# Kernel tuning notes

Hardware: AMD Instinct MI355X
Metric: run time of the kernel (lower is better)

The kernel has to match this reference:

```python
import jax, jax.numpy as jnp
from jax import lax
import numpy as np

TAU_R = 1.0
TAU_W = 5.0
W_MIN, W_MAX = 0.0, 0.05
N_MBON, N_FBN, N_DAN, N_KC = 20, 60, 20, 200
N_RECUR = N_MBON + N_FBN + N_DAN
B, T = 256, 61


def setup_inputs() -> dict:
    key = jax.random.key(0)
    ks = jax.random.split(key, 8)
    r_kc = jax.random.uniform(ks[0], (B, N_KC, T), dtype=jnp.float32)
    r_ext = jax.random.uniform(ks[1], (B, 2, T), dtype=jnp.float32)
    time = jnp.arange(T, dtype=jnp.float32) * 0.5  # dt = 0.5
    # KC->MBON plastic weights start at the max value (0.05), as in init
    W0_W = jax.random.uniform(ks[2], (B, N_MBON, N_KC), dtype=jnp.float32) * W_MAX
    W0_w = jax.random.uniform(ks[3], (B, N_MBON, N_KC), dtype=jnp.float32) * W_MAX
    sqrt2 = np.sqrt(2.0)
    W_mbon = jax.random.normal(ks[4], (N_RECUR, N_MBON)) * np.sqrt(1.0 / (sqrt2 * N_MBON))
    W_fbn = jax.random.normal(ks[5], (N_RECUR, N_FBN)) * np.sqrt(1.0 / (sqrt2 * N_FBN))
    W_dan = jax.random.normal(ks[6], (N_RECUR, N_DAN)) * np.sqrt(1.0 / (sqrt2 * N_DAN))
    W_recur = jnp.concatenate([W_mbon, W_fbn, W_dan], axis=1).astype(jnp.float32)
    W_ext = jax.random.normal(ks[7], (N_FBN, 2), dtype=jnp.float32)
    bias = jnp.full((N_RECUR,), 0.1, dtype=jnp.float32)
    W_readout = jax.random.normal(jax.random.fold_in(key, 99), (1, N_MBON), dtype=jnp.float32) / np.sqrt(N_MBON)
    return {"r_kc": r_kc, "r_ext": r_ext, "time": time, "n_batch": B,
            "W0_W": W0_W, "W0_w": W0_w, "W_recur": W_recur, "W_ext": W_ext,
            "bias": bias, "W_readout": W_readout}


def reference(r_kc, r_ext, time, n_batch, W0_W, W0_w, W_recur, W_ext, bias, W_readout):
    n_mbon, n_kc = W0_W.shape[1], W0_W.shape[2]
    n_fbn = W_ext.shape[0]
    n_recur = W_recur.shape[0]
    n_dan = n_recur - n_mbon - n_fbn
    nb = r_kc.shape[0]
    dt = time[1] - time[0]

    # initial state: FBN/DAN at 0.1, MBON at 0
    r_init = jnp.full((nb, n_recur), 0.1, dtype=r_kc.dtype).at[:, :n_mbon].set(0.0)
    # DAN->MBON weights are zeroed
    Wr = W_recur.at[:n_mbon, -n_dan:].set(0.0)
    rbk0 = r_kc[:, :, 0]            # KC eligibility trace
    rbd0 = r_init[:, -n_dan:]       # DAN eligibility trace
    readout0 = jnp.einsum('om,bm->bo', W_readout, r_init[:, :n_mbon]).squeeze(-1)
    zeros_dan = jnp.zeros((nb, n_dan), dtype=r_kc.dtype)

    def step(carry, xs):
        r, W, wt, rbk, rbd = carry
        rk_t, re_t = xs                                   # [B,n_kc], [B,n_ext]
        I_kc = jnp.einsum('bmk,bk->bm', W, rk_t)          # KC -> MBON via plastic W
        I_fbn = jnp.einsum('fe,be->bf', W_ext, re_t)      # context -> FBN
        I_tot = jnp.concatenate([I_kc, I_fbn, zeros_dan], axis=1)
        Wr_prod = jnp.einsum('sr,br->bs', Wr, r)
        dr = (-r + jax.nn.relu(Wr_prod + bias + I_tot)) / TAU_R
        r_new = r + dr * dt
        # plasticity update (uses the *new* DAN activity)
        rbk_new = rbk + (rk_t - rbk) * dt / TAU_W
        r_dan = r_new[:, -n_dan:]
        rbd_new = rbd + (r_dan - rbd) * dt / TAU_W
        dw = (jnp.einsum('bd,bk->bdk', rbd_new, rk_t)
              - jnp.einsum('bd,bk->bdk', r_dan, rbk_new))
        wt_new = wt + dw * dt
        W_new = jnp.clip(W + (-W + wt_new) / TAU_W * dt, W_MIN, W_MAX)
        ro = jnp.einsum('om,bm->bo', W_readout, r_new[:, :n_mbon]).squeeze(-1)
        return (r_new, W_new, wt_new, rbk_new, rbd_new), (r_new, W_new, wt_new, ro)

    xs = (jnp.moveaxis(r_kc, 2, 0)[:-1], jnp.moveaxis(r_ext, 2, 0)[:-1])
    carry0 = (r_init, W0_W, W0_w, rbk0, rbd0)
    _, (r_s, W_s, wt_s, ro_s) = lax.scan(step, carry0, xs)
    r_series = jnp.concatenate([r_init[None], r_s], axis=0)    # [T,B,n_recur]
    W_series = jnp.concatenate([W0_W[None], W_s], axis=0)      # [T,B,n_mbon,n_kc]
    wt_series = jnp.concatenate([W0_w[None], wt_s], axis=0)    # [T,B,n_mbon,n_kc]
    readout = jnp.concatenate([readout0[None], ro_s], axis=0)  # [T,B]
    return r_series, W_series, wt_series, readout
```

## Files before the change

kernel.cpp:

```cpp
#include <hip/hip_runtime.h>


#define NKC   200
#define NREC  100
#define TSTEP 61
#define NSTEP 60
#define WRSTR 108
#define PSTR  52
#define NTHR  512

typedef float vfloat4 __attribute__((ext_vector_type(4)));

__device__ __forceinline__ void bar_lds() {
    __builtin_amdgcn_sched_barrier(0);
    asm volatile("s_waitcnt lgkmcnt(0)");
    __builtin_amdgcn_s_barrier();
    __builtin_amdgcn_sched_barrier(0);
}

__device__ __forceinline__ void nt_store4(float* p, float4 v) {
    vfloat4 t;
    t.x = v.x; t.y = v.y; t.z = v.z; t.w = v.w;
    __builtin_nontemporal_store(t, (vfloat4*)p);
}
__device__ __forceinline__ void nt_store1(float* p, float v) {
    __builtin_nontemporal_store(v, p);
}

__global__ __launch_bounds__(NTHR, 1) void cond_rnn_kernel(
    const float* __restrict__ r_kc, const float* __restrict__ r_ext,
    const float* __restrict__ timev, const float* __restrict__ W0_W,
    const float* __restrict__ W0_w, const float* __restrict__ W_recur,
    const float* __restrict__ W_ext, const float* __restrict__ bias,
    const float* __restrict__ W_readout, float* __restrict__ out, int B)
{
    int b = blockIdx.x;
    if ((B & 7) == 0) {
        const int cpx = B >> 3;
        b = (blockIdx.x & 7) * cpx + (blockIdx.x >> 3);
    }
    const int tid = threadIdx.x;
    const float dt  = timev[1] - timev[0];
    const float dtw = dt / 5.0f;

    __shared__ __align__(16) float s_rk[TSTEP * NKC];
    __shared__ __align__(16) float s_re[128];
    __shared__ __align__(16) float s_Wr[NREC * WRSTR];
    __shared__ __align__(16) float s_Wro[32];
    __shared__ __align__(16) float s_r[2][112];
    __shared__ __align__(16) float s_rbd[32];
    __shared__ __align__(16) float s_part[20 * PSTR];

    const float* rk_b = r_kc + (size_t)b * (NKC * TSTEP);
    for (int f = tid; f < NKC * TSTEP; f += NTHR) {
        int k = f / TSTEP, t = f - k * TSTEP;
        s_rk[t * NKC + k] = rk_b[f];
    }
    const float* re_b = r_ext + (size_t)b * (2 * TSTEP);
    if (tid < 2 * TSTEP) s_re[tid] = re_b[tid];
    for (int f = tid; f < NREC * NREC; f += NTHR) {
        int s = f / NREC, j = f - s * NREC;
        float v = W_recur[f];
        if (s < 20 && j >= 80) v = 0.f;
        s_Wr[s * WRSTR + j] = v;
    }
    if (tid < 20)  s_Wro[tid] = W_readout[tid];
    if (tid < 100) s_r[0][tid] = (tid < 20) ? 0.f : 0.1f;
    if (tid < 20)  s_rbd[tid] = 0.1f;

    float my_bias = 0.f, we0 = 0.f, we1 = 0.f;
    if (tid < 100) my_bias = bias[tid];
    if (tid >= 20 && tid < 80) { we0 = W_ext[(tid - 20) * 2]; we1 = W_ext[(tid - 20) * 2 + 1]; }
    float rbd_mine = 0.1f;
    float r_mine   = (tid < 20) ? 0.f : 0.1f;

    float* out_r  = out;
    float* out_W  = out + (size_t)TSTEP * B * 100;
    float* out_wt = out_W + (size_t)TSTEP * B * 4000;
    float* out_ro = out_wt + (size_t)TSTEP * B * 4000;

    float4 Wreg[2], wtreg[2], rbkreg[2], rkc[2];
    const float* W0Wb = W0_W + (size_t)b * 4000;
    const float* W0wb = W0_w + (size_t)b * 4000;
    #pragma unroll
    for (int i = 0; i < 2; ++i) {
        int c = tid + NTHR * i;
        if (c < 1000) {
            Wreg[i]  = *(const float4*)(W0Wb + 4 * c);
            wtreg[i] = *(const float4*)(W0wb + 4 * c);
            nt_store4(out_W  + (size_t)b * 4000 + 4 * c, Wreg[i]);
            nt_store4(out_wt + (size_t)b * 4000 + 4 * c, wtreg[i]);
        }
    }
    if (tid < 100) nt_store1(out_r + (size_t)b * 100 + tid, r_mine);

    __syncthreads();

    #pragma unroll
    for (int i = 0; i < 2; ++i) {
        int c = tid + NTHR * i;
        if (c < 1000) {
            int k0 = (4 * c) % NKC;
            int m  = c / 50;
            float4 rk0 = *(const float4*)(s_rk + k0);
            rbkreg[i] = rk0;
            rkc[i]    = rk0;
            float4 w = Wreg[i];
            s_part[m * PSTR + (c % 50)] =
                w.x * rk0.x + w.y * rk0.y + w.z * rk0.z + w.w * rk0.w;
        }
    }
    if (tid == 255) {
        float ro = 0.f;
        #pragma unroll
        for (int mm = 0; mm < 20; ++mm) ro += s_Wro[mm] * s_r[0][mm];
        nt_store1(out_ro + b, ro);
    }
    __syncthreads();

    for (int it = 0; it < NSTEP; ++it) {
        const int cur = it & 1, nxt = cur ^ 1;

        if (tid < 100) {
            float acc = my_bias;
            if (tid < 20) {
                const float* pp = s_part + tid * PSTR;
                #pragma unroll
                for (int q4 = 0; q4 < 12; ++q4) {
                    float4 p4 = *(const float4*)(pp + 4 * q4);
                    acc += p4.x + p4.y + p4.z + p4.w;
                }
                acc += pp[48] + pp[49];
            } else if (tid < 80) {
                acc = fmaf(we0, s_re[it], acc);
                acc = fmaf(we1, s_re[TSTEP + it], acc);
            }
            const float* wr = s_Wr + tid * WRSTR;
            #pragma unroll
            for (int j4 = 0; j4 < 25; ++j4) {
                float4 w4 = *(const float4*)(wr + 4 * j4);
                float4 r4 = *(const float4*)(&s_r[cur][4 * j4]);
                acc = fmaf(w4.x, r4.x, acc); acc = fmaf(w4.y, r4.y, acc);
                acc = fmaf(w4.z, r4.z, acc); acc = fmaf(w4.w, r4.w, acc);
            }
            float drive = acc > 0.f ? acc : 0.f;
            float rn = r_mine + dt * (drive - r_mine);
            r_mine = rn;
            s_r[nxt][tid] = rn;
            nt_store1(out_r + (size_t)(it + 1) * B * 100 + (size_t)b * 100 + tid, rn);
            if (tid >= 80) {
                rbd_mine += (rn - rbd_mine) * dtw;
                s_rbd[tid - 80] = rbd_mine;
            }
        }
        bar_lds();

        float* oW  = out_W  + (size_t)(it + 1) * B * 4000 + (size_t)b * 4000;
        float* owt = out_wt + (size_t)(it + 1) * B * 4000 + (size_t)b * 4000;
        const float* rk_nx  = s_rk + (it + 1) * NKC;
        #pragma unroll
        for (int i = 0; i < 2; ++i) {
            int c = tid + NTHR * i;
            if (c < 1000) {
                int k0 = (4 * c) % NKC;
                int m  = c / 50;
                float4 rk4 = rkc[i];
                float4 rkn = *(const float4*)(rk_nx + k0);
                rkc[i] = rkn;
                float rbdn = s_rbd[m];
                float rdan = s_r[nxt][80 + m];
                float4 rb = rbkreg[i];
                rb.x += (rk4.x - rb.x) * dtw;  rb.y += (rk4.y - rb.y) * dtw;
                rb.z += (rk4.z - rb.z) * dtw;  rb.w += (rk4.w - rb.w) * dtw;
                rbkreg[i] = rb;
                float4 wt = wtreg[i];
                wt.x = fmaf(rbdn * rk4.x - rdan * rb.x, dt, wt.x);
                wt.y = fmaf(rbdn * rk4.y - rdan * rb.y, dt, wt.y);
                wt.z = fmaf(rbdn * rk4.z - rdan * rb.z, dt, wt.z);
                wt.w = fmaf(rbdn * rk4.w - rdan * rb.w, dt, wt.w);
                wtreg[i] = wt;
                float4 w = Wreg[i];
                w.x += (wt.x - w.x) * dtw;  w.y += (wt.y - w.y) * dtw;
                w.z += (wt.z - w.z) * dtw;  w.w += (wt.w - w.w) * dtw;
                w.x = fminf(fmaxf(w.x, 0.f), 0.05f);
                w.y = fminf(fmaxf(w.y, 0.f), 0.05f);
                w.z = fminf(fmaxf(w.z, 0.f), 0.05f);
                w.w = fminf(fmaxf(w.w, 0.f), 0.05f);
                Wreg[i] = w;
                s_part[m * PSTR + (c % 50)] =
                    w.x * rkn.x + w.y * rkn.y + w.z * rkn.z + w.w * rkn.w;
                nt_store4(owt + 4 * c, wt);
                nt_store4(oW  + 4 * c, w);
            }
        }
        if (tid == 255) {
            float ro = 0.f;
            #pragma unroll
            for (int mm = 0; mm < 20; ++mm) ro += s_Wro[mm] * s_r[nxt][mm];
            nt_store1(out_ro + (size_t)(it + 1) * B + b, ro);
        }
        bar_lds();
    }
}

extern "C" void kernel_launch(void* const* d_in, const int* in_sizes, int n_in,
                              void* d_out, int out_size, void* d_ws, size_t ws_size,
                              hipStream_t stream) {
    const float* r_kc      = (const float*)d_in[0];
    const float* r_ext     = (const float*)d_in[1];
    const float* timev     = (const float*)d_in[2];
    const float* W0_W      = (const float*)d_in[4];
    const float* W0_w      = (const float*)d_in[5];
    const float* W_recur   = (const float*)d_in[6];
    const float* W_ext     = (const float*)d_in[7];
    const float* bias      = (const float*)d_in[8];
    const float* W_readout = (const float*)d_in[9];

    const int B = in_sizes[0] / (NKC * TSTEP);
    cond_rnn_kernel<<<dim3(B), dim3(NTHR), 0, stream>>>(
        r_kc, r_ext, timev, W0_W, W0_w, W_recur, W_ext, bias, W_readout,
        (float*)d_out, B);
}
```

Baseline: 520.4 us.

## Duplicate per-batch recurrence across two blocks and stream r_kc through a ring buffer

Launches two blocks per batch element. Each block recomputes the full recurrence, but each writes only half of the W/wt output stores, which spreads the store bandwidth over more CUs. The full 61-step r_kc staging in LDS is replaced by a 24-row ring buffer that is refilled every 8 steps, so LDS use drops and up to 4 blocks per CU can be resident. The cost is doubled compute and doubled global reads, plus strided, uncoalesced refill loads inside the time loop.

```diff
diff --git a/kernel.cpp b/kernel.cpp
--- a/kernel.cpp
+++ b/kernel.cpp
@@ -8,6 +8,7 @@
 #define WRSTR 108
 #define PSTR  52
 #define NTHR  512
+#define WN    24
 
 typedef float vfloat4 __attribute__((ext_vector_type(4)));
 
@@ -27,23 +28,20 @@
     __builtin_nontemporal_store(v, p);
 }
 
-__global__ __launch_bounds__(NTHR, 1) void cond_rnn_kernel(
+__global__ __launch_bounds__(NTHR, 4) void cond_rnn_kernel(
     const float* __restrict__ r_kc, const float* __restrict__ r_ext,
     const float* __restrict__ timev, const float* __restrict__ W0_W,
     const float* __restrict__ W0_w, const float* __restrict__ W_recur,
     const float* __restrict__ W_ext, const float* __restrict__ bias,
     const float* __restrict__ W_readout, float* __restrict__ out, int B)
 {
-    int b = blockIdx.x;
-    if ((B & 7) == 0) {
-        const int cpx = B >> 3;
-        b = (blockIdx.x & 7) * cpx + (blockIdx.x >> 3);
-    }
+    const int b   = blockIdx.x >> 1;
+    const int h   = blockIdx.x & 1;
     const int tid = threadIdx.x;
     const float dt  = timev[1] - timev[0];
     const float dtw = dt / 5.0f;
 
-    __shared__ __align__(16) float s_rk[TSTEP * NKC];
+    __shared__ __align__(16) float s_rkw[WN * NKC];
     __shared__ __align__(16) float s_re[128];
     __shared__ __align__(16) float s_Wr[NREC * WRSTR];
     __shared__ __align__(16) float s_Wro[32];
@@ -52,9 +50,9 @@
     __shared__ __align__(16) float s_part[20 * PSTR];
 
     const float* rk_b = r_kc + (size_t)b * (NKC * TSTEP);
-    for (int f = tid; f < NKC * TSTEP; f += NTHR) {
-        int k = f / TSTEP, t = f - k * TSTEP;
-        s_rk[t * NKC + k] = rk_b[f];
+    for (int f = tid; f < WN * NKC; f += NTHR) {
+        int r = f / NKC, k = f - r * NKC;
+        s_rkw[r * NKC + k] = rk_b[k * TSTEP + r];
     }
     const float* re_b = r_ext + (size_t)b * (2 * TSTEP);
     if (tid < 2 * TSTEP) s_re[tid] = re_b[tid];
@@ -88,11 +86,13 @@
         if (c < 1000) {
             Wreg[i]  = *(const float4*)(W0Wb + 4 * c);
             wtreg[i] = *(const float4*)(W0wb + 4 * c);
-            nt_store4(out_W  + (size_t)b * 4000 + 4 * c, Wreg[i]);
-            nt_store4(out_wt + (size_t)b * 4000 + 4 * c, wtreg[i]);
-        }
-    }
-    if (tid < 100) nt_store1(out_r + (size_t)b * 100 + tid, r_mine);
+            if ((c < 500) == (h == 0)) {
+                nt_store4(out_W  + (size_t)b * 4000 + 4 * c, Wreg[i]);
+                nt_store4(out_wt + (size_t)b * 4000 + 4 * c, wtreg[i]);
+            }
+        }
+    }
+    if (h == 0 && tid < 100) nt_store1(out_r + (size_t)b * 100 + tid, r_mine);
 
     __syncthreads();
 
@@ -102,7 +102,7 @@
         if (c < 1000) {
             int k0 = (4 * c) % NKC;
             int m  = c / 50;
-            float4 rk0 = *(const float4*)(s_rk + k0);
+            float4 rk0 = *(const float4*)(s_rkw + k0);
             rbkreg[i] = rk0;
             rkc[i]    = rk0;
             float4 w = Wreg[i];
@@ -110,7 +110,7 @@
                 w.x * rk0.x + w.y * rk0.y + w.z * rk0.z + w.w * rk0.w;
         }
     }
-    if (tid == 255) {
+    if (h == 0 && tid == 255) {
         float ro = 0.f;
         #pragma unroll
         for (int mm = 0; mm < 20; ++mm) ro += s_Wro[mm] * s_r[0][mm];
@@ -147,17 +147,30 @@
             float rn = r_mine + dt * (drive - r_mine);
             r_mine = rn;
             s_r[nxt][tid] = rn;
-            nt_store1(out_r + (size_t)(it + 1) * B * 100 + (size_t)b * 100 + tid, rn);
+            if (h == 0)
+                nt_store1(out_r + (size_t)(it + 1) * B * 100 + (size_t)b * 100 + tid, rn);
             if (tid >= 80) {
                 rbd_mine += (rn - rbd_mine) * dtw;
                 s_rbd[tid - 80] = rbd_mine;
             }
         }
+
+        if ((it & 7) == 6) {
+            int t0 = it + 17;
+            int nrows = TSTEP - t0; if (nrows > 8) nrows = 8;
+            if (nrows > 0) {
+                for (int f = tid; f < nrows * NKC; f += NTHR) {
+                    int rr = f / NKC, k = f - rr * NKC;
+                    int t  = t0 + rr;
+                    s_rkw[(t % WN) * NKC + k] = rk_b[k * TSTEP + t];
+                }
+            }
+        }
         bar_lds();
 
         float* oW  = out_W  + (size_t)(it + 1) * B * 4000 + (size_t)b * 4000;
         float* owt = out_wt + (size_t)(it + 1) * B * 4000 + (size_t)b * 4000;
-        const float* rk_nx  = s_rk + (it + 1) * NKC;
+        const float* rk_nx = s_rkw + ((it + 1) % WN) * NKC;
         #pragma unroll
         for (int i = 0; i < 2; ++i) {
             int c = tid + NTHR * i;
@@ -189,11 +202,13 @@
                 Wreg[i] = w;
                 s_part[m * PSTR + (c % 50)] =
                     w.x * rkn.x + w.y * rkn.y + w.z * rkn.z + w.w * rkn.w;
-                nt_store4(owt + 4 * c, wt);
-                nt_store4(oW  + 4 * c, w);
-            }
-        }
-        if (tid == 255) {
+                if ((c < 500) == (h == 0)) {
+                    nt_store4(owt + 4 * c, wt);
+                    nt_store4(oW  + 4 * c, w);
+                }
+            }
+        }
+        if (h == 0 && tid == 255) {
             float ro = 0.f;
             #pragma unroll
             for (int mm = 0; mm < 20; ++mm) ro += s_Wro[mm] * s_r[nxt][mm];
@@ -217,7 +232,7 @@
     const float* W_readout = (const float*)d_in[9];
 
     const int B = in_sizes[0] / (NKC * TSTEP);
-    cond_rnn_kernel<<<dim3(B), dim3(NTHR), 0, stream>>>(
+    cond_rnn_kernel<<<dim3(2 * B), dim3(NTHR), 0, stream>>>(
         r_kc, r_ext, timev, W0_W, W0_w, W_recur, W_ext, bias, W_readout,
         (float*)d_out, B);
 }
```

After: 565.1 us. 8.6% more time.
